# Optimization experiments

Measured on AMD Instinct MI355X. Metric: run time of the kernel, lower is better.

Reference implementation:

```python
import jax, jax.numpy as jnp
import numpy as np

B, T, C = 512, 256, 192
HEAD = 64

def setup_inputs() -> dict:
    key = jax.random.key(0)
    ks = jax.random.split(key, 5)
    return {
        "x": jax.random.normal(ks[0], (B, T, C), dtype=jnp.float32),
        "Wk": jax.random.normal(ks[1], (C, HEAD), dtype=jnp.float32) * (C ** -0.5),
        "Wq": jax.random.normal(ks[2], (C, HEAD), dtype=jnp.float32) * (C ** -0.5),
        "Wv": jax.random.normal(ks[3], (C, HEAD), dtype=jnp.float32) * (C ** -0.5),
        "pos_table": jax.random.normal(ks[4], (T, C), dtype=jnp.float32),
    }

def reference(x, Wk, Wq, Wv, pos_table):
    Bx, Tx, Cx = x.shape
    scale = Cx ** -0.5  # note: scales by n_embed, not head_size (faithful to source)
    k = jnp.einsum('btc,ch->bth', x, Wk)
    q = jnp.einsum('btc,ch->bth', x, Wq)
    v = jnp.einsum('btc,ch->bth', x, Wv)
    pe = pos_table[:Tx]                       # [T, C]
    pos_k = pe @ Wk                           # [T, H]
    pos_q = pe @ Wq                           # [T, H]
    bias = pos_k @ pos_q.T                    # [T, T]
    wei = jnp.einsum('bqh,bkh->bqk', q, k) * scale + bias
    causal = jnp.tril(jnp.ones((Tx, Tx), dtype=bool))
    wei = jnp.where(causal, wei, -jnp.inf)
    wei = jax.nn.softmax(wei, axis=-1)
    # dropout is identity in inference mode
    out = jnp.einsum('bqk,bkh->bqh', wei, v)
    return out
```

## Files before the change

### kernel.cpp

```cpp
#include <hip/hip_runtime.h>
#include <hip/hip_bf16.h>

typedef unsigned short u16;
typedef unsigned int u32;
using bf16x8 = __attribute__((ext_vector_type(8))) short;
using f32x4  = __attribute__((ext_vector_type(4))) float;

#define BB 512
#define TT 256
#define CC 192
#define HH 64

__device__ __forceinline__ u16 f2bf(float f) {
    __hip_bfloat16 h = __float2bfloat16(f);
    u16 u; __builtin_memcpy(&u, &h, 2); return u;
}


__global__ void wprep_kernel(const float* __restrict__ Wq,
                             const float* __restrict__ Wk,
                             const float* __restrict__ Wv,
                             u16* __restrict__ W_sw) {
    int gid  = blockIdx.x * 256 + threadIdx.x;
    int fid  = gid >> 6, lane = gid & 63;
    int n3   = fid / 6,  ks   = fid % 6;
    int l15  = lane & 15, quad = lane >> 4;
    const float* W = (n3 < 4) ? Wq : (n3 < 8) ? Wk : Wv;
    const int h = (n3 & 3) * 16 + l15;
    u16* dst = W_sw + (size_t)gid * 8;
    #pragma unroll
    for (int u = 0; u < 8; ++u) {
        int c = ks * 32 + quad * 8 + u;
        dst[u] = f2bf(W[c * HH + h]);
    }
}

__global__ void pos_kernel(const float* __restrict__ Wk,
                           const float* __restrict__ Wq,
                           const float* __restrict__ pe,
                           float* __restrict__ poskT, float* __restrict__ posqT) {
    int t = blockIdx.x * 4 + (threadIdx.x >> 6);
    int h = threadIdx.x & 63;
    float ak = 0.f, aq = 0.f;
    for (int c = 0; c < CC; ++c) {
        float p = pe[t * CC + c];
        ak += p * Wk[c * HH + h];
        aq += p * Wq[c * HH + h];
    }
    poskT[h * TT + t] = ak;
    posqT[h * TT + t] = aq;
}

__global__ void bias_kernel(const float* __restrict__ poskT,
                            const float* __restrict__ posqT,
                            float4* __restrict__ bias_sw) {
    const int i = blockIdx.x >> 4, jt = blockIdx.x & 15;
    if (jt > i) return;
    const int lane = threadIdx.x;
    const int l15 = lane & 15, quad = lane >> 4;
    const int tq = i * 16 + quad * 4;
    const int jc = jt * 16 + l15;
    float s[4] = {0.f, 0.f, 0.f, 0.f};
    for (int h = 0; h < HH; ++h) {
        float pq = posqT[h * TT + jc];
        #pragma unroll
        for (int r = 0; r < 4; ++r)
            s[r] += poskT[h * TT + tq + r] * pq;
    }
    bias_sw[blockIdx.x * 64 + lane] = make_float4(s[0], s[1], s[2], s[3]);
}

#define XP 200

__global__ __launch_bounds__(256, 3)
void qkv_kernel(const float* __restrict__ x,
                const u16* __restrict__ W_sw,
                u16* __restrict__ q_sw, u16* __restrict__ k_sw,
                u16* __restrict__ vg) {
    __shared__ __align__(16) u16 xs[64 * XP];
    const int tid  = threadIdx.x;
    const int w    = tid >> 6;
    const int lane = tid & 63;
    const int l15  = lane & 15;
    const int quad = lane >> 4;
    const int b    = blockIdx.x >> 2;
    const int rb   = blockIdx.x & 3;
    const float* xb = x + ((size_t)b * TT + rb * 64) * CC;

    const bf16x8* Wv8 = (const bf16x8*)W_sw;
    bf16x8 Wf[18];
    #pragma unroll
    for (int mat = 0; mat < 3; ++mat)
        #pragma unroll
        for (int ks = 0; ks < 6; ++ks)
            Wf[mat * 6 + ks] = Wv8[(((mat * 4 + w) * 6) + ks) * 64 + lane];

    #pragma unroll
    for (int it = 0; it < 12; ++it) {
        const int flat = (it * 256 + tid) * 4;
        const int row = flat / CC, col = flat % CC;
        const float4 v = *(const float4*)(xb + flat);
        uint2 pk;
        pk.x = (u32)f2bf(v.x) | ((u32)f2bf(v.y) << 16);
        pk.y = (u32)f2bf(v.z) | ((u32)f2bf(v.w) << 16);
        *(uint2*)&xs[row * XP + col] = pk;
    }
    __syncthreads();

    f32x4 acc[12];
    #pragma unroll
    for (int i = 0; i < 12; ++i) acc[i] = {0.f, 0.f, 0.f, 0.f};
    #pragma unroll
    for (int ks = 0; ks < 6; ++ks) {
        bf16x8 a[4];
        #pragma unroll
        for (int m = 0; m < 4; ++m)
            a[m] = *(const bf16x8*)&xs[(m * 16 + l15) * XP + ks * 32 + quad * 8];
        #pragma unroll
        for (int m = 0; m < 4; ++m)
            #pragma unroll
            for (int mat = 0; mat < 3; ++mat)
                acc[m * 3 + mat] = __builtin_amdgcn_mfma_f32_16x16x32_bf16(
                    a[m], Wf[mat * 6 + ks], acc[m * 3 + mat], 0, 0, 0);
    }

    const int hs    = w >> 1;
    const int quadp = (w * 2 + (l15 >> 3)) & 3;
    const int u     = l15 & 7;
    #pragma unroll
    for (int m = 0; m < 4; ++m) {
        const int i_loc  = rb * 4 + m;
        const size_t bi  = (size_t)b * 16 + i_loc;
        const size_t base = (bi * 2 + hs) * 512 + (quadp * 16 + quad * 4) * 8 + u;
        #pragma unroll
        for (int r = 0; r < 4; ++r) {
            q_sw[base + r * 8] = f2bf(acc[m * 3 + 0][r]);
            k_sw[base + r * 8] = f2bf(acc[m * 3 + 1][r]);
        }
        const size_t t_glob = (size_t)b * TT + i_loc * 16;
        #pragma unroll
        for (int r = 0; r < 4; ++r)
            vg[(t_glob + quad * 4 + r) * HH + w * 16 + l15] = f2bf(acc[m * 3 + 2][r]);
    }
}

#define VP 264
#define PP 40
#define VT_ELEMS (HH * VP)
#define P_ELEMS 640
#define LDSB_ELEMS (VT_ELEMS + 4 * P_ELEMS)

__global__ __launch_bounds__(256, 4)
void attn_kernel(const u16* __restrict__ q_sw, const u16* __restrict__ k_sw,
                 const u16* __restrict__ vg, const float4* __restrict__ bias_sw,
                 float* __restrict__ out) {
    __shared__ __align__(16) u16 lds[LDSB_ELEMS];
    const int tid  = threadIdx.x;
    const int w    = tid >> 6;
    const int lane = tid & 63;
    const int l15  = lane & 15;
    const int quad = lane >> 4;
    const int b    = blockIdx.x >> 1;
    const int half = blockIdx.x & 1;

    {
        const u16* vrow = vg + ((size_t)b * TT + tid) * HH;
        #pragma unroll
        for (int u2 = 0; u2 < 8; ++u2) {
            bf16x8 vv = *(const bf16x8*)(vrow + u2 * 8);
            #pragma unroll
            for (int e = 0; e < 8; ++e)
                lds[(u2 * 8 + e) * VP + tid] = (u16)vv[e];
        }
    }
    __syncthreads();

    u16* Pw = &lds[VT_ELEMS + w * P_ELEMS];
    const float scale = 0.07216878364870322f;
    const f32x4 zero4 = {0.f, 0.f, 0.f, 0.f};
    const bf16x8* qv = (const bf16x8*)q_sw;
    const bf16x8* kv = (const bf16x8*)k_sw;

    #pragma unroll 1
    for (int mt = 0; mt < 2; ++mt) {
        const int i  = half ? (mt ? 11 - w : 4 + w) : (mt ? 15 - w : w);
        const int t0 = 16 * i;
        const int J  = i + 1;
        const int Pq = (J + 1) >> 1;
        const size_t bi = (size_t)b * 16 + i;

        const bf16x8 qf0 = qv[(bi * 2 + 0) * 64 + lane];
        const bf16x8 qf1 = qv[(bi * 2 + 1) * 64 + lane];

        f32x4 o[4];
        float m4[4], l4[4];
        #pragma unroll
        for (int n = 0; n < 4; ++n) o[n] = zero4;
        #pragma unroll
        for (int r = 0; r < 4; ++r) { m4[r] = -1e30f; l4[r] = 0.f; }

        #pragma unroll
        for (int p = 0; p < 8; ++p) {
            if (p < Pq) {
                const int jt0 = 2 * p, jt1 = 2 * p + 1;
                f32x4 sa = zero4, sb;
                {
                    const size_t bj = (size_t)b * 16 + jt0;
                    bf16x8 k0 = kv[(bj * 2 + 0) * 64 + lane];
                    bf16x8 k1 = kv[(bj * 2 + 1) * 64 + lane];
                    sa = __builtin_amdgcn_mfma_f32_16x16x32_bf16(qf0, k0, sa, 0, 0, 0);
                    sa = __builtin_amdgcn_mfma_f32_16x16x32_bf16(qf1, k1, sa, 0, 0, 0);
                    const float4 b4 = bias_sw[(i * 16 + jt0) * 64 + lane];
                    sa[0] = sa[0] * scale + b4.x;
                    sa[1] = sa[1] * scale + b4.y;
                    sa[2] = sa[2] * scale + b4.z;
                    sa[3] = sa[3] * scale + b4.w;
                    if (jt0 == i) {
                        #pragma unroll
                        for (int r = 0; r < 4; ++r)
                            if (l15 > quad * 4 + r) sa[r] = -1e30f;
                    }
                }
                if (jt1 < J) {
                    sb = zero4;
                    const size_t bj = (size_t)b * 16 + jt1;
                    bf16x8 k0 = kv[(bj * 2 + 0) * 64 + lane];
                    bf16x8 k1 = kv[(bj * 2 + 1) * 64 + lane];
                    sb = __builtin_amdgcn_mfma_f32_16x16x32_bf16(qf0, k0, sb, 0, 0, 0);
                    sb = __builtin_amdgcn_mfma_f32_16x16x32_bf16(qf1, k1, sb, 0, 0, 0);
                    const float4 b4 = bias_sw[(i * 16 + jt1) * 64 + lane];
                    sb[0] = sb[0] * scale + b4.x;
                    sb[1] = sb[1] * scale + b4.y;
                    sb[2] = sb[2] * scale + b4.z;
                    sb[3] = sb[3] * scale + b4.w;
                    if (jt1 == i) {
                        #pragma unroll
                        for (int r = 0; r < 4; ++r)
                            if (l15 > quad * 4 + r) sb[r] = -1e30f;
                    }
                } else {
                    sb[0] = -1e30f; sb[1] = -1e30f; sb[2] = -1e30f; sb[3] = -1e30f;
                }
                float t4[4];
                #pragma unroll
                for (int r = 0; r < 4; ++r) t4[r] = fmaxf(sa[r], sb[r]);
                #pragma unroll
                for (int d = 1; d < 16; d <<= 1) {
                    #pragma unroll
                    for (int r = 0; r < 4; ++r) t4[r] = fmaxf(t4[r], __shfl_xor(t4[r], d, 64));
                }
                float al[4];
                #pragma unroll
                for (int r = 0; r < 4; ++r) {
                    float mn = fmaxf(m4[r], t4[r]);
                    al[r] = __expf(m4[r] - mn);
                    m4[r] = mn;
                    l4[r] *= al[r];
                }
                #pragma unroll
                for (int n = 0; n < 4; ++n)
                #pragma unroll
                for (int r = 0; r < 4; ++r) o[n][r] *= al[r];
                #pragma unroll
                for (int r = 0; r < 4; ++r) {
                    float e0 = __expf(sa[r] - m4[r]);
                    float e1 = __expf(sb[r] - m4[r]);
                    l4[r] += e0 + e1;
                    Pw[(quad * 4 + r) * PP + l15]      = f2bf(e0);
                    Pw[(quad * 4 + r) * PP + 16 + l15] = f2bf(e1);
                }
                bf16x8 pa = *(const bf16x8*)&Pw[l15 * PP + quad * 8];
                #pragma unroll
                for (int n = 0; n < 4; ++n) {
                    bf16x8 bv = *(const bf16x8*)&lds[(n * 16 + l15) * VP + p * 32 + quad * 8];
                    o[n] = __builtin_amdgcn_mfma_f32_16x16x32_bf16(pa, bv, o[n], 0, 0, 0);
                }
            }
        }
        #pragma unroll
        for (int d = 1; d < 16; d <<= 1) {
            #pragma unroll
            for (int r = 0; r < 4; ++r) l4[r] += __shfl_xor(l4[r], d, 64);
        }
        float rl4[4];
        #pragma unroll
        for (int r = 0; r < 4; ++r) rl4[r] = 1.f / l4[r];
        float* ob = out + ((size_t)b * TT + t0) * HH;
        #pragma unroll
        for (int n = 0; n < 4; ++n)
        #pragma unroll
        for (int r = 0; r < 4; ++r)
            ob[(quad * 4 + r) * HH + n * 16 + l15] = o[n][r] * rl4[r];
    }
}

extern "C" void kernel_launch(void* const* d_in, const int* in_sizes, int n_in,
                              void* d_out, int out_size, void* d_ws, size_t ws_size,
                              hipStream_t stream) {
    const float* x  = (const float*)d_in[0];
    const float* Wk = (const float*)d_in[1];
    const float* Wq = (const float*)d_in[2];
    const float* Wv = (const float*)d_in[3];
    const float* pe = (const float*)d_in[4];
    float* out = (float*)d_out;

    float*  poskT  = (float*)d_ws;
    float*  posqT  = poskT + TT * HH;
    float4* biassw = (float4*)(posqT + TT * HH);
    u16*    W_sw   = (u16*)((float*)biassw + TT * TT);
    u16*    q_sw   = W_sw + 3 * HH * CC;
    u16*    k_sw   = q_sw + (size_t)BB * TT * HH;
    u16*    vg     = k_sw + (size_t)BB * TT * HH;

    wprep_kernel<<<18, 256, 0, stream>>>(Wq, Wk, Wv, W_sw);
    pos_kernel<<<TT / 4, 256, 0, stream>>>(Wk, Wq, pe, poskT, posqT);
    bias_kernel<<<256, 64, 0, stream>>>(poskT, posqT, biassw);
    qkv_kernel<<<4 * BB, 256, 0, stream>>>(x, W_sw, q_sw, k_sw, vg);
    attn_kernel<<<2 * BB, 256, 0, stream>>>(q_sw, k_sw, vg, biassw, out);
}
```

Before: 219.2 us.

## Load x via async global-to-LDS with swizzle and prefetch next K/bias tiles

In the QKV projection kernel, x is now copied directly from global memory into LDS as fp32 using global_load_lds with an XOR swizzle. The bf16 conversion moves to the point where MFMA operands are read, so the weight-register loads can overlap the x copy. This doubles the LDS footprint (64x192 floats), which may reduce occupancy. In the attention kernel, the next pair of K fragments and bias tiles are prefetched into registers one iteration ahead to hide global load latency, at the cost of extra registers.

Result: slower. 246.7 us (+12.6%).

```diff
diff --git a/kernel.cpp b/kernel.cpp
--- a/kernel.cpp
+++ b/kernel.cpp
@@ -70,14 +70,13 @@
     bias_sw[blockIdx.x * 64 + lane] = make_float4(s[0], s[1], s[2], s[3]);
 }
 
-#define XP 200
 
 __global__ __launch_bounds__(256, 3)
 void qkv_kernel(const float* __restrict__ x,
                 const u16* __restrict__ W_sw,
                 u16* __restrict__ q_sw, u16* __restrict__ k_sw,
                 u16* __restrict__ vg) {
-    __shared__ __align__(16) u16 xs[64 * XP];
+    __shared__ __align__(16) float xs[64 * CC];
     const int tid  = threadIdx.x;
     const int w    = tid >> 6;
     const int lane = tid & 63;
@@ -85,7 +84,18 @@
     const int quad = lane >> 4;
     const int b    = blockIdx.x >> 2;
     const int rb   = blockIdx.x & 3;
-    const float* xb = x + ((size_t)b * TT + rb * 64) * CC;
+    const char* xb = (const char*)(x + ((size_t)b * TT + rb * 64) * CC);
+
+    #pragma unroll
+    for (int it = 0; it < 12; ++it) {
+        const int o = w * 12288 + it * 1024 + lane * 16;
+        const int r = o / 768;
+        const int c = (o % 768) ^ ((r & 7) << 4);
+        __builtin_amdgcn_global_load_lds(
+            (const __attribute__((address_space(1))) void*)(xb + r * 768 + c),
+            (__attribute__((address_space(3))) void*)((char*)xs + w * 12288 + it * 1024),
+            16, 0, 0);
+    }
 
     const bf16x8* Wv8 = (const bf16x8*)W_sw;
     bf16x8 Wf[18];
@@ -95,16 +105,6 @@
         for (int ks = 0; ks < 6; ++ks)
             Wf[mat * 6 + ks] = Wv8[(((mat * 4 + w) * 6) + ks) * 64 + lane];
 
-    #pragma unroll
-    for (int it = 0; it < 12; ++it) {
-        const int flat = (it * 256 + tid) * 4;
-        const int row = flat / CC, col = flat % CC;
-        const float4 v = *(const float4*)(xb + flat);
-        uint2 pk;
-        pk.x = (u32)f2bf(v.x) | ((u32)f2bf(v.y) << 16);
-        pk.y = (u32)f2bf(v.z) | ((u32)f2bf(v.w) << 16);
-        *(uint2*)&xs[row * XP + col] = pk;
-    }
     __syncthreads();
 
     f32x4 acc[12];
@@ -114,8 +114,20 @@
     for (int ks = 0; ks < 6; ++ks) {
         bf16x8 a[4];
         #pragma unroll
-        for (int m = 0; m < 4; ++m)
-            a[m] = *(const bf16x8*)&xs[(m * 16 + l15) * XP + ks * 32 + quad * 8];
+        for (int m = 0; m < 4; ++m) {
+            const int row = m * 16 + l15;
+            const int sw  = (row & 7) << 4;
+            const int cb  = ks * 128 + quad * 32;
+            const char* base = (const char*)xs + row * 768;
+            const float4 f0 = *(const float4*)(base + ((cb     ) ^ sw));
+            const float4 f1 = *(const float4*)(base + ((cb + 16) ^ sw));
+            bf16x8 av;
+            av[0] = (short)f2bf(f0.x); av[1] = (short)f2bf(f0.y);
+            av[2] = (short)f2bf(f0.z); av[3] = (short)f2bf(f0.w);
+            av[4] = (short)f2bf(f1.x); av[5] = (short)f2bf(f1.y);
+            av[6] = (short)f2bf(f1.z); av[7] = (short)f2bf(f1.w);
+            a[m] = av;
+        }
         #pragma unroll
         for (int m = 0; m < 4; ++m)
             #pragma unroll
@@ -199,18 +211,37 @@
         #pragma unroll
         for (int r = 0; r < 4; ++r) { m4[r] = -1e30f; l4[r] = 0.f; }
 
+        bf16x8 kc[4]; float4 bcf[2];
+        {
+            const size_t bj = (size_t)b * 32;
+            kc[0] = kv[(bj + 0) * 64 + lane];
+            kc[1] = kv[(bj + 1) * 64 + lane];
+            kc[2] = kv[(bj + 2) * 64 + lane];
+            kc[3] = kv[(bj + 3) * 64 + lane];
+            bcf[0] = bias_sw[(i * 16 + 0) * 64 + lane];
+            bcf[1] = bias_sw[(i * 16 + 1) * 64 + lane];
+        }
+
         #pragma unroll
         for (int p = 0; p < 8; ++p) {
             if (p < Pq) {
                 const int jt0 = 2 * p, jt1 = 2 * p + 1;
+                bf16x8 kn[4]; float4 bnf[2];
+                const bool hn = (p + 1 < Pq);
+                if (hn) {
+                    const size_t bj = ((size_t)b * 16 + 2 * p + 2) * 2;
+                    kn[0] = kv[(bj + 0) * 64 + lane];
+                    kn[1] = kv[(bj + 1) * 64 + lane];
+                    kn[2] = kv[(bj + 2) * 64 + lane];
+                    kn[3] = kv[(bj + 3) * 64 + lane];
+                    bnf[0] = bias_sw[(i * 16 + 2 * p + 2) * 64 + lane];
+                    bnf[1] = bias_sw[(i * 16 + 2 * p + 3) * 64 + lane];
+                }
                 f32x4 sa = zero4, sb;
                 {
-                    const size_t bj = (size_t)b * 16 + jt0;
-                    bf16x8 k0 = kv[(bj * 2 + 0) * 64 + lane];
-                    bf16x8 k1 = kv[(bj * 2 + 1) * 64 + lane];
-                    sa = __builtin_amdgcn_mfma_f32_16x16x32_bf16(qf0, k0, sa, 0, 0, 0);
-                    sa = __builtin_amdgcn_mfma_f32_16x16x32_bf16(qf1, k1, sa, 0, 0, 0);
-                    const float4 b4 = bias_sw[(i * 16 + jt0) * 64 + lane];
+                    sa = __builtin_amdgcn_mfma_f32_16x16x32_bf16(qf0, kc[0], sa, 0, 0, 0);
+                    sa = __builtin_amdgcn_mfma_f32_16x16x32_bf16(qf1, kc[1], sa, 0, 0, 0);
+                    const float4 b4 = bcf[0];
                     sa[0] = sa[0] * scale + b4.x;
                     sa[1] = sa[1] * scale + b4.y;
                     sa[2] = sa[2] * scale + b4.z;
@@ -223,12 +254,9 @@
                 }
                 if (jt1 < J) {
                     sb = zero4;
-                    const size_t bj = (size_t)b * 16 + jt1;
-                    bf16x8 k0 = kv[(bj * 2 + 0) * 64 + lane];
-                    bf16x8 k1 = kv[(bj * 2 + 1) * 64 + lane];
-                    sb = __builtin_amdgcn_mfma_f32_16x16x32_bf16(qf0, k0, sb, 0, 0, 0);
-                    sb = __builtin_amdgcn_mfma_f32_16x16x32_bf16(qf1, k1, sb, 0, 0, 0);
-                    const float4 b4 = bias_sw[(i * 16 + jt1) * 64 + lane];
+                    sb = __builtin_amdgcn_mfma_f32_16x16x32_bf16(qf0, kc[2], sb, 0, 0, 0);
+                    sb = __builtin_amdgcn_mfma_f32_16x16x32_bf16(qf1, kc[3], sb, 0, 0, 0);
+                    const float4 b4 = bcf[1];
                     sb[0] = sb[0] * scale + b4.x;
                     sb[1] = sb[1] * scale + b4.y;
                     sb[2] = sb[2] * scale + b4.z;
@@ -275,6 +303,10 @@
                     bf16x8 bv = *(const bf16x8*)&lds[(n * 16 + l15) * VP + p * 32 + quad * 8];
                     o[n] = __builtin_amdgcn_mfma_f32_16x16x32_bf16(pa, bv, o[n], 0, 0, 0);
                 }
+                if (hn) {
+                    kc[0] = kn[0]; kc[1] = kn[1]; kc[2] = kn[2]; kc[3] = kn[3];
+                    bcf[0] = bnf[0]; bcf[1] = bnf[1];
+                }
             }
         }
         #pragma unroll
```

## Load x tile directly into LDS as fp32 with XOR swizzle, convert on read

Applied to the files above, without the earlier changes.

The qkv kernel now stages the x tile into shared memory with direct global-to-LDS loads in fp32, using an XOR swizzle on 16-byte chunks per row, instead of loading into registers, converting to bf16 and storing. The loads are issued before the weight-fragment loads, so the two can overlap. Conversion to bf16 moves into the MFMA operand read, with two float4 LDS reads per fragment. LDS use doubles to 48KB per block, which may reduce occupancy under launch_bounds(256,3), and the conversion is now redone per fragment read.

Result: no change. 220.2 us (+0.5%).

```diff
diff --git a/kernel.cpp b/kernel.cpp
--- a/kernel.cpp
+++ b/kernel.cpp
@@ -70,14 +70,13 @@
     bias_sw[blockIdx.x * 64 + lane] = make_float4(s[0], s[1], s[2], s[3]);
 }
 
-#define XP 200
 
 __global__ __launch_bounds__(256, 3)
 void qkv_kernel(const float* __restrict__ x,
                 const u16* __restrict__ W_sw,
                 u16* __restrict__ q_sw, u16* __restrict__ k_sw,
                 u16* __restrict__ vg) {
-    __shared__ __align__(16) u16 xs[64 * XP];
+    __shared__ __align__(16) float xs[64 * CC];
     const int tid  = threadIdx.x;
     const int w    = tid >> 6;
     const int lane = tid & 63;
@@ -85,7 +84,18 @@
     const int quad = lane >> 4;
     const int b    = blockIdx.x >> 2;
     const int rb   = blockIdx.x & 3;
-    const float* xb = x + ((size_t)b * TT + rb * 64) * CC;
+    const char* xb = (const char*)(x + ((size_t)b * TT + rb * 64) * CC);
+
+    #pragma unroll
+    for (int it = 0; it < 12; ++it) {
+        const int o = w * 12288 + it * 1024 + lane * 16;
+        const int r = o / 768;
+        const int c = (o % 768) ^ ((r & 7) << 4);
+        __builtin_amdgcn_global_load_lds(
+            (const __attribute__((address_space(1))) void*)(xb + r * 768 + c),
+            (__attribute__((address_space(3))) void*)((char*)xs + w * 12288 + it * 1024),
+            16, 0, 0);
+    }
 
     const bf16x8* Wv8 = (const bf16x8*)W_sw;
     bf16x8 Wf[18];
@@ -95,16 +105,6 @@
         for (int ks = 0; ks < 6; ++ks)
             Wf[mat * 6 + ks] = Wv8[(((mat * 4 + w) * 6) + ks) * 64 + lane];
 
-    #pragma unroll
-    for (int it = 0; it < 12; ++it) {
-        const int flat = (it * 256 + tid) * 4;
-        const int row = flat / CC, col = flat % CC;
-        const float4 v = *(const float4*)(xb + flat);
-        uint2 pk;
-        pk.x = (u32)f2bf(v.x) | ((u32)f2bf(v.y) << 16);
-        pk.y = (u32)f2bf(v.z) | ((u32)f2bf(v.w) << 16);
-        *(uint2*)&xs[row * XP + col] = pk;
-    }
     __syncthreads();
 
     f32x4 acc[12];
@@ -114,8 +114,20 @@
     for (int ks = 0; ks < 6; ++ks) {
         bf16x8 a[4];
         #pragma unroll
-        for (int m = 0; m < 4; ++m)
-            a[m] = *(const bf16x8*)&xs[(m * 16 + l15) * XP + ks * 32 + quad * 8];
+        for (int m = 0; m < 4; ++m) {
+            const int row = m * 16 + l15;
+            const int sw  = (row & 7) << 4;
+            const int cb  = ks * 128 + quad * 32;
+            const char* base = (const char*)xs + row * 768;
+            const float4 f0 = *(const float4*)(base + ((cb     ) ^ sw));
+            const float4 f1 = *(const float4*)(base + ((cb + 16) ^ sw));
+            bf16x8 av;
+            av[0] = (short)f2bf(f0.x); av[1] = (short)f2bf(f0.y);
+            av[2] = (short)f2bf(f0.z); av[3] = (short)f2bf(f0.w);
+            av[4] = (short)f2bf(f1.x); av[5] = (short)f2bf(f1.y);
+            av[6] = (short)f2bf(f1.z); av[7] = (short)f2bf(f1.w);
+            a[m] = av;
+        }
         #pragma unroll
         for (int m = 0; m < 4; ++m)
             #pragma unroll
```

## Fuse QKV projection and causal attention into one per-batch kernel using LDS

Applied to the files above, without the earlier changes.

Merges the QKV projection and attention kernels into a single kernel where each block handles one batch. It computes Q, K and V in 32-row chunks directly into shared memory, then runs attention over all 16 query tiles. This removes the global-memory write and read-back of the bf16 Q, K and V intermediates and one kernel launch. In exchange each block needs about 112 KB of dynamic LDS and runs with one block per CU, which cuts occupancy and serializes projection and attention within a block.

After: 216.0 us. Within noise of the previous version (-1.4%).

```diff
diff --git a/kernel.cpp b/kernel.cpp
--- a/kernel.cpp
+++ b/kernel.cpp
@@ -70,22 +70,33 @@
     bias_sw[blockIdx.x * 64 + lane] = make_float4(s[0], s[1], s[2], s[3]);
 }
 
+
 #define XP 200
-
-__global__ __launch_bounds__(256, 3)
-void qkv_kernel(const float* __restrict__ x,
-                const u16* __restrict__ W_sw,
-                u16* __restrict__ q_sw, u16* __restrict__ k_sw,
-                u16* __restrict__ vg) {
-    __shared__ __align__(16) u16 xs[64 * XP];
+#define VP 264
+#define PP 40
+#define P_ELEMS 640
+#define Q_OFF 12800
+#define K_OFF 45568
+#define V_OFF 78336
+#define LDS_TOTAL 112128
+
+__global__ __launch_bounds__(256, 1)
+void fused_kernel(const float* __restrict__ x,
+                  const u16* __restrict__ W_sw,
+                  const float4* __restrict__ bias_sw,
+                  float* __restrict__ out) {
+    extern __shared__ __align__(16) char smem[];
+    u16* xs   = (u16*)smem;
+    u16* Qlds = (u16*)(smem + Q_OFF);
+    u16* Klds = (u16*)(smem + K_OFF);
+    u16* Vt   = (u16*)(smem + V_OFF);
+
     const int tid  = threadIdx.x;
     const int w    = tid >> 6;
     const int lane = tid & 63;
     const int l15  = lane & 15;
     const int quad = lane >> 4;
-    const int b    = blockIdx.x >> 2;
-    const int rb   = blockIdx.x & 3;
-    const float* xb = x + ((size_t)b * TT + rb * 64) * CC;
+    const int b    = blockIdx.x;
 
     const bf16x8* Wv8 = (const bf16x8*)W_sw;
     bf16x8 Wf[18];
@@ -94,103 +105,76 @@
         #pragma unroll
         for (int ks = 0; ks < 6; ++ks)
             Wf[mat * 6 + ks] = Wv8[(((mat * 4 + w) * 6) + ks) * 64 + lane];
-
-    #pragma unroll
-    for (int it = 0; it < 12; ++it) {
-        const int flat = (it * 256 + tid) * 4;
-        const int row = flat / CC, col = flat % CC;
-        const float4 v = *(const float4*)(xb + flat);
-        uint2 pk;
-        pk.x = (u32)f2bf(v.x) | ((u32)f2bf(v.y) << 16);
-        pk.y = (u32)f2bf(v.z) | ((u32)f2bf(v.w) << 16);
-        *(uint2*)&xs[row * XP + col] = pk;
-    }
-    __syncthreads();
-
-    f32x4 acc[12];
-    #pragma unroll
-    for (int i = 0; i < 12; ++i) acc[i] = {0.f, 0.f, 0.f, 0.f};
-    #pragma unroll
-    for (int ks = 0; ks < 6; ++ks) {
-        bf16x8 a[4];
-        #pragma unroll
-        for (int m = 0; m < 4; ++m)
-            a[m] = *(const bf16x8*)&xs[(m * 16 + l15) * XP + ks * 32 + quad * 8];
-        #pragma unroll
-        for (int m = 0; m < 4; ++m)
-            #pragma unroll
-            for (int mat = 0; mat < 3; ++mat)
-                acc[m * 3 + mat] = __builtin_amdgcn_mfma_f32_16x16x32_bf16(
-                    a[m], Wf[mat * 6 + ks], acc[m * 3 + mat], 0, 0, 0);
-    }
+    __builtin_amdgcn_sched_barrier(0);
 
     const int hs    = w >> 1;
     const int quadp = (w * 2 + (l15 >> 3)) & 3;
-    const int u     = l15 & 7;
-    #pragma unroll
-    for (int m = 0; m < 4; ++m) {
-        const int i_loc  = rb * 4 + m;
-        const size_t bi  = (size_t)b * 16 + i_loc;
-        const size_t base = (bi * 2 + hs) * 512 + (quadp * 16 + quad * 4) * 8 + u;
-        #pragma unroll
-        for (int r = 0; r < 4; ++r) {
-            q_sw[base + r * 8] = f2bf(acc[m * 3 + 0][r]);
-            k_sw[base + r * 8] = f2bf(acc[m * 3 + 1][r]);
-        }
-        const size_t t_glob = (size_t)b * TT + i_loc * 16;
-        #pragma unroll
-        for (int r = 0; r < 4; ++r)
-            vg[(t_glob + quad * 4 + r) * HH + w * 16 + l15] = f2bf(acc[m * 3 + 2][r]);
-    }
-}
-
-#define VP 264
-#define PP 40
-#define VT_ELEMS (HH * VP)
-#define P_ELEMS 640
-#define LDSB_ELEMS (VT_ELEMS + 4 * P_ELEMS)
-
-__global__ __launch_bounds__(256, 4)
-void attn_kernel(const u16* __restrict__ q_sw, const u16* __restrict__ k_sw,
-                 const u16* __restrict__ vg, const float4* __restrict__ bias_sw,
-                 float* __restrict__ out) {
-    __shared__ __align__(16) u16 lds[LDSB_ELEMS];
-    const int tid  = threadIdx.x;
-    const int w    = tid >> 6;
-    const int lane = tid & 63;
-    const int l15  = lane & 15;
-    const int quad = lane >> 4;
-    const int b    = blockIdx.x >> 1;
-    const int half = blockIdx.x & 1;
-
-    {
-        const u16* vrow = vg + ((size_t)b * TT + tid) * HH;
-        #pragma unroll
-        for (int u2 = 0; u2 < 8; ++u2) {
-            bf16x8 vv = *(const bf16x8*)(vrow + u2 * 8);
-            #pragma unroll
-            for (int e = 0; e < 8; ++e)
-                lds[(u2 * 8 + e) * VP + tid] = (u16)vv[e];
-        }
-    }
-    __syncthreads();
-
-    u16* Pw = &lds[VT_ELEMS + w * P_ELEMS];
+    const int uu    = l15 & 7;
+
+    #pragma unroll 1
+    for (int c8 = 0; c8 < 8; ++c8) {
+        const float* xb = x + ((size_t)b * TT + c8 * 32) * CC;
+        #pragma unroll
+        for (int it = 0; it < 6; ++it) {
+            const int flat = (it * 256 + tid) * 4;
+            const int row = flat / CC, col = flat % CC;
+            const float4 v = *(const float4*)(xb + flat);
+            uint2 pk;
+            pk.x = (u32)f2bf(v.x) | ((u32)f2bf(v.y) << 16);
+            pk.y = (u32)f2bf(v.z) | ((u32)f2bf(v.w) << 16);
+            *(uint2*)&xs[row * XP + col] = pk;
+        }
+        __syncthreads();
+
+        f32x4 acc[6];
+        #pragma unroll
+        for (int i = 0; i < 6; ++i) acc[i] = {0.f, 0.f, 0.f, 0.f};
+        #pragma unroll
+        for (int ks = 0; ks < 6; ++ks) {
+            bf16x8 a[2];
+            #pragma unroll
+            for (int m = 0; m < 2; ++m)
+                a[m] = *(const bf16x8*)&xs[(m * 16 + l15) * XP + ks * 32 + quad * 8];
+            #pragma unroll
+            for (int m = 0; m < 2; ++m)
+                #pragma unroll
+                for (int mat = 0; mat < 3; ++mat)
+                    acc[m * 3 + mat] = __builtin_amdgcn_mfma_f32_16x16x32_bf16(
+                        a[m], Wf[mat * 6 + ks], acc[m * 3 + mat], 0, 0, 0);
+        }
+
+        #pragma unroll
+        for (int m = 0; m < 2; ++m) {
+            const int i_loc = c8 * 2 + m;
+            const int base  = (i_loc * 2 + hs) * 512 + (quadp * 16 + quad * 4) * 8 + uu;
+            #pragma unroll
+            for (int r = 0; r < 4; ++r) {
+                Qlds[base + r * 8] = f2bf(acc[m * 3 + 0][r]);
+                Klds[base + r * 8] = f2bf(acc[m * 3 + 1][r]);
+            }
+            #pragma unroll
+            for (int r = 0; r < 4; ++r)
+                Vt[(w * 16 + l15) * VP + i_loc * 16 + quad * 4 + r]
+                    = f2bf(acc[m * 3 + 2][r]);
+        }
+        __syncthreads();
+    }
+
+    u16* Pw = (u16*)smem + w * P_ELEMS;
     const float scale = 0.07216878364870322f;
     const f32x4 zero4 = {0.f, 0.f, 0.f, 0.f};
-    const bf16x8* qv = (const bf16x8*)q_sw;
-    const bf16x8* kv = (const bf16x8*)k_sw;
+    const bf16x8* qv = (const bf16x8*)Qlds;
+    const bf16x8* kv = (const bf16x8*)Klds;
 
     #pragma unroll 1
-    for (int mt = 0; mt < 2; ++mt) {
-        const int i  = half ? (mt ? 11 - w : 4 + w) : (mt ? 15 - w : w);
+    for (int mt = 0; mt < 4; ++mt) {
+        const int i = (mt == 0) ? w : (mt == 1) ? 15 - w : (mt == 2) ? 4 + w : 11 - w;
         const int t0 = 16 * i;
         const int J  = i + 1;
         const int Pq = (J + 1) >> 1;
-        const size_t bi = (size_t)b * 16 + i;
-
-        const bf16x8 qf0 = qv[(bi * 2 + 0) * 64 + lane];
-        const bf16x8 qf1 = qv[(bi * 2 + 1) * 64 + lane];
+
+        const bf16x8 qf0 = qv[(i * 2 + 0) * 64 + lane];
+        const bf16x8 qf1 = qv[(i * 2 + 1) * 64 + lane];
 
         f32x4 o[4];
         float m4[4], l4[4];
@@ -205,9 +189,8 @@
                 const int jt0 = 2 * p, jt1 = 2 * p + 1;
                 f32x4 sa = zero4, sb;
                 {
-                    const size_t bj = (size_t)b * 16 + jt0;
-                    bf16x8 k0 = kv[(bj * 2 + 0) * 64 + lane];
-                    bf16x8 k1 = kv[(bj * 2 + 1) * 64 + lane];
+                    bf16x8 k0 = kv[(jt0 * 2 + 0) * 64 + lane];
+                    bf16x8 k1 = kv[(jt0 * 2 + 1) * 64 + lane];
                     sa = __builtin_amdgcn_mfma_f32_16x16x32_bf16(qf0, k0, sa, 0, 0, 0);
                     sa = __builtin_amdgcn_mfma_f32_16x16x32_bf16(qf1, k1, sa, 0, 0, 0);
                     const float4 b4 = bias_sw[(i * 16 + jt0) * 64 + lane];
@@ -223,9 +206,8 @@
                 }
                 if (jt1 < J) {
                     sb = zero4;
-                    const size_t bj = (size_t)b * 16 + jt1;
-                    bf16x8 k0 = kv[(bj * 2 + 0) * 64 + lane];
-                    bf16x8 k1 = kv[(bj * 2 + 1) * 64 + lane];
+                    bf16x8 k0 = kv[(jt1 * 2 + 0) * 64 + lane];
+                    bf16x8 k1 = kv[(jt1 * 2 + 1) * 64 + lane];
                     sb = __builtin_amdgcn_mfma_f32_16x16x32_bf16(qf0, k0, sb, 0, 0, 0);
                     sb = __builtin_amdgcn_mfma_f32_16x16x32_bf16(qf1, k1, sb, 0, 0, 0);
                     const float4 b4 = bias_sw[(i * 16 + jt1) * 64 + lane];
@@ -272,7 +254,7 @@
                 bf16x8 pa = *(const bf16x8*)&Pw[l15 * PP + quad * 8];
                 #pragma unroll
                 for (int n = 0; n < 4; ++n) {
-                    bf16x8 bv = *(const bf16x8*)&lds[(n * 16 + l15) * VP + p * 32 + quad * 8];
+                    bf16x8 bv = *(const bf16x8*)&Vt[(n * 16 + l15) * VP + p * 32 + quad * 8];
                     o[n] = __builtin_amdgcn_mfma_f32_16x16x32_bf16(pa, bv, o[n], 0, 0, 0);
                 }
             }
@@ -308,13 +290,16 @@
     float*  posqT  = poskT + TT * HH;
     float4* biassw = (float4*)(posqT + TT * HH);
     u16*    W_sw   = (u16*)((float*)biassw + TT * TT);
-    u16*    q_sw   = W_sw + 3 * HH * CC;
-    u16*    k_sw   = q_sw + (size_t)BB * TT * HH;
-    u16*    vg     = k_sw + (size_t)BB * TT * HH;
+
+    static bool attr_set = false;
+    if (!attr_set) {
+        hipFuncSetAttribute(reinterpret_cast<const void*>(fused_kernel),
+                            hipFuncAttributeMaxDynamicSharedMemorySize, LDS_TOTAL);
+        attr_set = true;
+    }
 
     wprep_kernel<<<18, 256, 0, stream>>>(Wq, Wk, Wv, W_sw);
     pos_kernel<<<TT / 4, 256, 0, stream>>>(Wk, Wq, pe, poskT, posqT);
     bias_kernel<<<256, 64, 0, stream>>>(poskT, posqT, biassw);
-    qkv_kernel<<<4 * BB, 256, 0, stream>>>(x, W_sw, q_sw, k_sw, vg);
-    attn_kernel<<<2 * BB, 256, 0, stream>>>(q_sw, k_sw, vg, biassw, out);
-}
+    fused_kernel<<<BB, 256, LDS_TOTAL, stream>>>(x, W_sw, biassw, out);
+}
```
